# Performance work log

Hardware: AMD Instinct MI355X
Metric: run time of the kernel (lower is better)

The kernel has to match this reference:

```python
import jax, jax.numpy as jnp
import numpy as np

L = 192                      # lattice side
N = L ** 3                   # N_wells = 7,077,888


def _lattice_neighbors():
    """Periodic 6-neighbor stencil indices on an L^3 lattice."""
    idx = np.arange(N, dtype=np.int64).reshape(L, L, L)
    roll = lambda ax, s: np.roll(idx, s, axis=ax).reshape(-1)
    return (roll(0, 1), roll(0, -1),   # x +/- 
            roll(1, 1), roll(1, -1),   # y +/- 
            roll(2, 1), roll(2, -1))   # z +/- 


def setup_inputs() -> dict:
    key = jax.random.key(0)
    ks = jax.random.split(key, 5)
    nx1, nx2, ny1, ny2, nz1, nz2 = _lattice_neighbors()
    return {
        "t": jnp.asarray([0.1], dtype=jnp.float32),
        "y": jax.random.normal(ks[0], (2 * N,), dtype=jnp.float32),
        "J": jnp.full((N,), 1.0, dtype=jnp.float32),
        "anisotropy": jnp.full((N,), 0.45, dtype=jnp.float32),
        "gamma": jnp.full((N,), 0.05, dtype=jnp.float32),
        "h_dis_x": 0.01 * jax.random.normal(ks[1], (N,), dtype=jnp.float32),
        "h_dis_y": 0.01 * jax.random.normal(ks[2], (N,), dtype=jnp.float32),
        "beta": jnp.full((N,), 0.01, dtype=jnp.float32),
        "e_disorder": 0.1 * jax.random.normal(ks[3], (N,), dtype=jnp.float32),
        "nn_idx_1": jnp.asarray(nx1), "nn_idx_2": jnp.asarray(nx2),
        "nn_idy_1": jnp.asarray(ny1), "nn_idy_2": jnp.asarray(ny2),
        "nn_idz_1": jnp.asarray(nz1), "nn_idz_2": jnp.asarray(nz2),
    }


def reference(t, y, J, anisotropy, gamma, h_dis_x, h_dis_y, beta, e_disorder,
              nn_idx_1, nn_idx_2, nn_idy_1, nn_idy_2, nn_idz_1, nn_idz_2):
    # temperature_dependent_rate == 0 branch (static relaxation RHS)
    n = y.shape[0] // 2
    x, p = y[:n], y[n:]

    def stencil(v):  # J * (sum of 4 in-plane neighbors + anisotropy * 2 z-neighbors)
        return J * (v[nn_idx_1] + v[nn_idx_2] + v[nn_idy_1] + v[nn_idy_2]
                    + anisotropy * (v[nn_idz_1] + v[nn_idz_2]))

    xL = stencil(x)
    yL = stencil(p)
    r2 = x * x + p * p                 # |psi|^2
    cross = xL * p - yL * x

    dx = gamma * p * cross + e_disorder * p - yL + h_dis_y + beta * r2 * p
    dp = -gamma * x * cross - e_disorder * x + xL - h_dis_x - beta * r2 * x
    return jnp.concatenate([dx, dp], axis=0)
```

## Files before the change

### kernel.cpp

```cpp
#include <hip/hip_runtime.h>


#define LDIM 192
#define LSQ  (LDIM * LDIM)
#define NTOT (LDIM * LDIM * LDIM)

__global__ __launch_bounds__(256) void dgpe_kernel(
    const float* __restrict__ y,
    const float* __restrict__ Jarr,
    const float* __restrict__ aniso,
    const float* __restrict__ gam,
    const float* __restrict__ hdx,
    const float* __restrict__ hdy,
    const float* __restrict__ beta,
    const float* __restrict__ edis,
    float* __restrict__ out)
{
    const int i = blockIdx.x * blockDim.x + threadIdx.x;
    if (i >= NTOT) return;

    const float* __restrict__ x = y;
    const float* __restrict__ p = y + NTOT;

    const unsigned ui  = (unsigned)i;
    const unsigned a   = ui / LSQ;
    const unsigned rem = ui - a * LSQ;
    const unsigned b   = rem / LDIM;
    const unsigned c   = rem - b * LDIM;

    const int xm = (a == 0)        ? i + (LDIM - 1) * LSQ  : i - LSQ;
    const int xp = (a == LDIM - 1) ? i - (LDIM - 1) * LSQ  : i + LSQ;
    const int ym = (b == 0)        ? i + (LDIM - 1) * LDIM : i - LDIM;
    const int yp = (b == LDIM - 1) ? i - (LDIM - 1) * LDIM : i + LDIM;
    const int zm = (c == 0)        ? i + (LDIM - 1)        : i - 1;
    const int zp = (c == LDIM - 1) ? i - (LDIM - 1)        : i + 1;

    const float Ji = Jarr[i];
    const float an = aniso[i];
    const float xi = x[i];
    const float pi = p[i];

    const float xL = Ji * (x[xm] + x[xp] + x[ym] + x[yp] + an * (x[zm] + x[zp]));
    const float yL = Ji * (p[xm] + p[xp] + p[ym] + p[yp] + an * (p[zm] + p[zp]));

    const float g  = gam[i];
    const float ed = edis[i];
    const float bt = beta[i];

    const float r2    = xi * xi + pi * pi;
    const float cross = xL * pi - yL * xi;

    const float dx =  g * pi * cross + ed * pi - yL + hdy[i] + bt * r2 * pi;
    const float dp = -g * xi * cross - ed * xi + xL - hdx[i] - bt * r2 * xi;

    out[i]        = dx;
    out[i + NTOT] = dp;
}

extern "C" void kernel_launch(void* const* d_in, const int* in_sizes, int n_in,
                              void* d_out, int out_size, void* d_ws, size_t ws_size,
                              hipStream_t stream) {
    const float* y_    = (const float*)d_in[1];
    const float* Jarr  = (const float*)d_in[2];
    const float* aniso = (const float*)d_in[3];
    const float* gam   = (const float*)d_in[4];
    const float* hdx   = (const float*)d_in[5];
    const float* hdy   = (const float*)d_in[6];
    const float* beta  = (const float*)d_in[7];
    const float* edis  = (const float*)d_in[8];
    float* out = (float*)d_out;

    const int threads = 256;
    const int blocks  = NTOT / threads;
    dgpe_kernel<<<blocks, threads, 0, stream>>>(y_, Jarr, aniso, gam, hdx, hdy,
                                                beta, edis, out);
}
```

Baseline: 355.0 us.

## Vectorize stencil to float4 per thread and remap blocks across XCDs

Each thread now computes four consecutive z-sites using 128-bit vector loads for the center, x/y neighbours and all per-site coefficient arrays, with z-neighbours built from in-register shuffles plus two scalar halo loads. Block IDs are remapped so consecutive logical blocks land on the same XCD, improving L2 reuse of the x/y-plane neighbours. This cuts the number of memory instructions and the index arithmetic. It relies on the lattice side being divisible by 4 and on the block count dividing evenly by the XCD count.

```diff
diff --git a/kernel.cpp b/kernel.cpp
--- a/kernel.cpp
+++ b/kernel.cpp
@@ -4,6 +4,12 @@
 #define LDIM 192
 #define LSQ  (LDIM * LDIM)
 #define NTOT (LDIM * LDIM * LDIM)
+#define NQ   (NTOT / 4)
+#define NBLK (NQ / 256)
+#define XCDS 8
+#define BPX  (NBLK / XCDS)
+
+typedef float f4 __attribute__((ext_vector_type(4)));
 
 __global__ __launch_bounds__(256) void dgpe_kernel(
     const float* __restrict__ y,
@@ -16,45 +22,69 @@
     const float* __restrict__ edis,
     float* __restrict__ out)
 {
-    const int i = blockIdx.x * blockDim.x + threadIdx.x;
-    if (i >= NTOT) return;
+    const int pb = blockIdx.x;
+    const int lb = (pb & (XCDS - 1)) * BPX + (pb >> 3);
+    const int t  = lb * 256 + threadIdx.x;
+    const int i  = t * 4;
 
-    const float* __restrict__ x = y;
-    const float* __restrict__ p = y + NTOT;
-
-    const unsigned ui  = (unsigned)i;
-    const unsigned a   = ui / LSQ;
-    const unsigned rem = ui - a * LSQ;
-    const unsigned b   = rem / LDIM;
-    const unsigned c   = rem - b * LDIM;
+    const unsigned ut  = (unsigned)t;
+    const unsigned r   = ut / 48u;
+    const unsigned c4  = (ut - r * 48u) * 4u;
+    const unsigned a   = r / 192u;
+    const unsigned b   = r - a * 192u;
 
     const int xm = (a == 0)        ? i + (LDIM - 1) * LSQ  : i - LSQ;
     const int xp = (a == LDIM - 1) ? i - (LDIM - 1) * LSQ  : i + LSQ;
     const int ym = (b == 0)        ? i + (LDIM - 1) * LDIM : i - LDIM;
     const int yp = (b == LDIM - 1) ? i - (LDIM - 1) * LDIM : i + LDIM;
-    const int zm = (c == 0)        ? i + (LDIM - 1)        : i - 1;
-    const int zp = (c == LDIM - 1) ? i - (LDIM - 1)        : i + 1;
+    const int rowbase = i - (int)c4;
+    const int zmi = (c4 == 0)   ? rowbase + (LDIM - 1) : i - 1;
+    const int zpi = (c4 == 188) ? rowbase              : i + 4;
 
-    const float Ji = Jarr[i];
-    const float an = aniso[i];
-    const float xi = x[i];
-    const float pi = p[i];
+    const float* __restrict__ x = y;
+    const float* __restrict__ p = y + NTOT;
 
-    const float xL = Ji * (x[xm] + x[xp] + x[ym] + x[yp] + an * (x[zm] + x[zp]));
-    const float yL = Ji * (p[xm] + p[xp] + p[ym] + p[yp] + an * (p[zm] + p[zp]));
+    const f4 xc  = *(const f4*)(x + i);
+    const f4 xxm = *(const f4*)(x + xm);
+    const f4 xxp = *(const f4*)(x + xp);
+    const f4 xym = *(const f4*)(x + ym);
+    const f4 xyp = *(const f4*)(x + yp);
+    const float xzm = x[zmi];
+    const float xzp = x[zpi];
 
-    const float g  = gam[i];
-    const float ed = edis[i];
-    const float bt = beta[i];
+    const f4 pc  = *(const f4*)(p + i);
+    const f4 pxm = *(const f4*)(p + xm);
+    const f4 pxp = *(const f4*)(p + xp);
+    const f4 pym = *(const f4*)(p + ym);
+    const f4 pyp = *(const f4*)(p + yp);
+    const float pzm = p[zmi];
+    const float pzp = p[zpi];
 
-    const float r2    = xi * xi + pi * pi;
-    const float cross = xL * pi - yL * xi;
+    const f4 J  = *(const f4*)(Jarr  + i);
+    const f4 an = *(const f4*)(aniso + i);
+    const f4 g  = *(const f4*)(gam   + i);
+    const f4 hx = *(const f4*)(hdx   + i);
+    const f4 hy = *(const f4*)(hdy   + i);
+    const f4 bt = *(const f4*)(beta  + i);
+    const f4 ed = *(const f4*)(edis  + i);
 
-    const float dx =  g * pi * cross + ed * pi - yL + hdy[i] + bt * r2 * pi;
-    const float dp = -g * xi * cross - ed * xi + xL - hdx[i] - bt * r2 * xi;
+    f4 xz, pz;
+    xz.x = xzm  + xc.y;  xz.y = xc.x + xc.z;
+    xz.z = xc.y + xc.w;  xz.w = xc.z + xzp;
+    pz.x = pzm  + pc.y;  pz.y = pc.x + pc.z;
+    pz.z = pc.y + pc.w;  pz.w = pc.z + pzp;
 
-    out[i]        = dx;
-    out[i + NTOT] = dp;
+    const f4 xL = J * ((xxm + xxp + xym + xyp) + an * xz);
+    const f4 yL = J * ((pxm + pxp + pym + pyp) + an * pz);
+
+    const f4 r2    = xc * xc + pc * pc;
+    const f4 cross = xL * pc - yL * xc;
+
+    const f4 dx =  g * pc * cross + ed * pc - yL + hy + bt * r2 * pc;
+    const f4 dp = -(g * xc * cross) - ed * xc + xL - hx - bt * r2 * xc;
+
+    *(f4*)(out + i)        = dx;
+    *(f4*)(out + NTOT + i) = dp;
 }
 
 extern "C" void kernel_launch(void* const* d_in, const int* in_sizes, int n_in,
@@ -70,8 +100,6 @@
     const float* edis  = (const float*)d_in[8];
     float* out = (float*)d_out;
 
-    const int threads = 256;
-    const int blocks  = NTOT / threads;
-    dgpe_kernel<<<blocks, threads, 0, stream>>>(y_, Jarr, aniso, gam, hdx, hdy,
-                                                beta, edis, out);
+    dgpe_kernel<<<NBLK, 256, 0, stream>>>(y_, Jarr, aniso, gam, hdx, hdy,
+                                          beta, edis, out);
 }
```

After: 362.9 us. +2.2%, slower.

## Vectorize stencil to float4 along z and march rows in y with register reuse

Applied to the files above, without the earlier changes.

Each thread now handles four contiguous z-points with float4 loads and stores and walks four consecutive y-rows. It keeps the previous, current and next rows in registers so y-neighbours are not reloaded. This cuts the number of memory instructions and redundant neighbour loads relative to one thread per point. In exchange it uses more registers per thread, launches fewer threads, and needs extra scalar loads at the z-chunk edges.

```diff
diff --git a/kernel.cpp b/kernel.cpp
--- a/kernel.cpp
+++ b/kernel.cpp
@@ -4,8 +4,15 @@
 #define LDIM 192
 #define LSQ  (LDIM * LDIM)
 #define NTOT (LDIM * LDIM * LDIM)
+#define HSTEP 4
+#define ZCH  (LDIM / 4)
+#define YGRP (LDIM / HSTEP)
+#define NTHREADS (LDIM * YGRP * ZCH)
+#define NBLK (NTHREADS / 256)
 
-__global__ __launch_bounds__(256) void dgpe_kernel(
+typedef float f4 __attribute__((ext_vector_type(4)));
+
+__global__ __launch_bounds__(256, 4) void dgpe_kernel(
     const float* __restrict__ y,
     const float* __restrict__ Jarr,
     const float* __restrict__ aniso,
@@ -16,45 +23,87 @@
     const float* __restrict__ edis,
     float* __restrict__ out)
 {
-    const int i = blockIdx.x * blockDim.x + threadIdx.x;
-    if (i >= NTOT) return;
+    const int t = blockIdx.x * 256 + threadIdx.x;
+
+    const unsigned ut = (unsigned)t;
+    const unsigned zc = ut % 48u;
+    const unsigned r  = ut / 48u;
+    const unsigned yg = r % 48u;
+    const unsigned a  = r / 48u;
+
+    const int c4 = (int)zc * 4;
+    const int b0 = (int)yg * HSTEP;
+    const int aL = (int)a * LSQ;
+
+    const int zmo = (c4 == 0)          ? (LDIM - 1)  : -1;
+    const int zpo = (c4 == LDIM - 4)   ? -(LDIM - 4) : 4;
+
+    const int am = (a == 0)        ? (LDIM - 1) : (int)a - 1;
+    const int ap = (a == LDIM - 1) ? 0          : (int)a + 1;
+    int xmi = am * LSQ + b0 * LDIM + c4;
+    int xpi = ap * LSQ + b0 * LDIM + c4;
 
     const float* __restrict__ x = y;
     const float* __restrict__ p = y + NTOT;
 
-    const unsigned ui  = (unsigned)i;
-    const unsigned a   = ui / LSQ;
-    const unsigned rem = ui - a * LSQ;
-    const unsigned b   = rem / LDIM;
-    const unsigned c   = rem - b * LDIM;
+    const int bm  = (b0 == 0) ? (LDIM - 1) : (b0 - 1);
+    const int iym = aL + bm * LDIM + c4;
+    f4 ymx = *(const f4*)(x + iym);
+    f4 ymp = *(const f4*)(p + iym);
 
-    const int xm = (a == 0)        ? i + (LDIM - 1) * LSQ  : i - LSQ;
-    const int xp = (a == LDIM - 1) ? i - (LDIM - 1) * LSQ  : i + LSQ;
-    const int ym = (b == 0)        ? i + (LDIM - 1) * LDIM : i - LDIM;
-    const int yp = (b == LDIM - 1) ? i - (LDIM - 1) * LDIM : i + LDIM;
-    const int zm = (c == 0)        ? i + (LDIM - 1)        : i - 1;
-    const int zp = (c == LDIM - 1) ? i - (LDIM - 1)        : i + 1;
+    int ib = aL + b0 * LDIM + c4;
+    f4 cx = *(const f4*)(x + ib);  float cxzm = x[ib + zmo], cxzp = x[ib + zpo];
+    f4 cp = *(const f4*)(p + ib);  float cpzm = p[ib + zmo], cpzp = p[ib + zpo];
 
-    const float Ji = Jarr[i];
-    const float an = aniso[i];
-    const float xi = x[i];
-    const float pi = p[i];
+#pragma unroll
+    for (int k = 0; k < HSTEP; ++k) {
+        const int b  = b0 + k;
+        int bn = b + 1; if (bn == LDIM) bn = 0;
+        const int inx = aL + bn * LDIM + c4;
 
-    const float xL = Ji * (x[xm] + x[xp] + x[ym] + x[yp] + an * (x[zm] + x[zp]));
-    const float yL = Ji * (p[xm] + p[xp] + p[ym] + p[yp] + an * (p[zm] + p[zp]));
+        const f4  nx   = *(const f4*)(x + inx);
+        const float nxzm = x[inx + zmo], nxzp = x[inx + zpo];
+        const f4  np   = *(const f4*)(p + inx);
+        const float npzm = p[inx + zmo], npzp = p[inx + zpo];
 
-    const float g  = gam[i];
-    const float ed = edis[i];
-    const float bt = beta[i];
+        const f4 xmx = *(const f4*)(x + xmi);
+        const f4 xpx = *(const f4*)(x + xpi);
+        const f4 xmp = *(const f4*)(p + xmi);
+        const f4 xpp = *(const f4*)(p + xpi);
 
-    const float r2    = xi * xi + pi * pi;
-    const float cross = xL * pi - yL * xi;
+        const f4 J  = *(const f4*)(Jarr  + ib);
+        const f4 an = *(const f4*)(aniso + ib);
+        const f4 g  = *(const f4*)(gam   + ib);
+        const f4 hx = *(const f4*)(hdx   + ib);
+        const f4 hy = *(const f4*)(hdy   + ib);
+        const f4 bt = *(const f4*)(beta  + ib);
+        const f4 ed = *(const f4*)(edis  + ib);
 
-    const float dx =  g * pi * cross + ed * pi - yL + hdy[i] + bt * r2 * pi;
-    const float dp = -g * xi * cross - ed * xi + xL - hdx[i] - bt * r2 * xi;
+        f4 xz, pz;
+        xz.x = cxzm + cx.y;  xz.y = cx.x + cx.z;
+        xz.z = cx.y + cx.w;  xz.w = cx.z + cxzp;
+        pz.x = cpzm + cp.y;  pz.y = cp.x + cp.z;
+        pz.z = cp.y + cp.w;  pz.w = cp.z + cpzp;
 
-    out[i]        = dx;
-    out[i + NTOT] = dp;
+        const f4 xL = J * ((xmx + xpx + ymx + nx) + an * xz);
+        const f4 yL = J * ((xmp + xpp + ymp + np) + an * pz);
+
+        const f4 r2    = cx * cx + cp * cp;
+        const f4 cross = xL * cp - yL * cx;
+
+        const f4 dx =  g * cp * cross + ed * cp - yL + hy + bt * r2 * cp;
+        const f4 dp = -(g * cx * cross) - ed * cx + xL - hx - bt * r2 * cx;
+
+        *(f4*)(out + ib)        = dx;
+        *(f4*)(out + NTOT + ib) = dp;
+
+        ymx = cx;  ymp = cp;
+        cx = nx;   cxzm = nxzm;  cxzp = nxzp;
+        cp = np;   cpzm = npzm;  cpzp = npzp;
+        ib  += LDIM;
+        xmi += LDIM;
+        xpi += LDIM;
+    }
 }
 
 extern "C" void kernel_launch(void* const* d_in, const int* in_sizes, int n_in,
@@ -70,8 +119,6 @@
     const float* edis  = (const float*)d_in[8];
     float* out = (float*)d_out;
 
-    const int threads = 256;
-    const int blocks  = NTOT / threads;
-    dgpe_kernel<<<blocks, threads, 0, stream>>>(y_, Jarr, aniso, gam, hdx, hdy,
-                                                beta, edis, out);
+    dgpe_kernel<<<NBLK, 256, 0, stream>>>(y_, Jarr, aniso, gam, hdx, hdy,
+                                          beta, edis, out);
 }
```

Result: slower. 366.6 us (+3.3%).
